# Kernel optimization log

Hardware: AMD Instinct MI355X
Metric: run time of the kernel (lower is better)

Reference implementation:

```python
import jax, jax.numpy as jnp
import numpy as np

B, S, H, N = 512, 50, 512, 20000


def setup_inputs() -> dict:
    key = jax.random.key(0)
    ks = jax.random.split(key, 8)
    sc = 1.0 / np.sqrt(H)
    return {
        "all_memory": jax.random.normal(ks[0], (B, S, H), jnp.float32),
        "last_memory": jax.random.normal(ks[1], (B, H), jnp.float32),
        "item_seq": jax.random.randint(ks[2], (B, S), 0, N),
        "mask": jnp.zeros((B, S), dtype=bool),
        "U_w": jax.random.normal(ks[3], (H, H), jnp.float32) * sc,
        "W_w": jax.random.normal(ks[4], (H, H), jnp.float32) * sc,
        "V_w": jax.random.normal(ks[5], (H,), jnp.float32) * sc,
        "V_b": jnp.zeros((1,), jnp.float32),
        "E_w": jax.random.normal(ks[6], (N, 2 * H), jnp.float32) * sc,
    }


def reference(all_memory, last_memory, item_seq, mask, U_w, W_w, V_w, V_b, E_w):
    # Additive (Bahdanau) attention over the basket-sequence memory.
    # torch nn.Linear computes x @ W.T (dropout is identity at eval).
    am = jnp.einsum('bsh,kh->bsk', all_memory, U_w)          # U_explore(all_memory)
    lm = last_memory @ W_w.T                                  # W_explore(last_memory)
    scores = jnp.tanh(am + lm[:, None, :]) @ V_w + V_b[0]     # [B, S]
    scores = jnp.where(mask, -1e9, scores)                    # masked_fill_
    alpha = jax.nn.softmax(scores, axis=1)                    # softmax over seq dim
    ctx = jnp.einsum('bs,bsh->bh', alpha, all_memory)         # attention readout
    feat = jnp.concatenate([ctx, last_memory], axis=-1)       # [B, 2H]
    logits = feat @ E_w.T                                     # [B, N] big GEMM
    # explore_mask = bmm((item_seq>0), one_hot(item_seq)) == scatter-add of counts
    counts = jnp.zeros((B, N), jnp.float32).at[
        jnp.arange(B)[:, None], item_seq
    ].add((item_seq > 0).astype(jnp.float32))
    logits = jnp.where(counts > 0, -jnp.inf, logits)          # mask seen items
    return jax.nn.sigmoid(logits)                             # sigmoid(-inf) -> 0
```

## Files before the change

### kernel.cpp

```cpp
#include <hip/hip_runtime.h>
#include <hip/hip_bf16.h>

#define Bdim 512
#define Sdim 50
#define Hdim 512
#define Ndim 20000
#define Kdim2 1024
#define SEENW 640

typedef __bf16 bf16x8 __attribute__((ext_vector_type(8)));
typedef float f32x4 __attribute__((ext_vector_type(4)));
typedef unsigned short u16;

__device__ __forceinline__ u16 f2bf(float f) {
  unsigned u = __builtin_bit_cast(unsigned, f);
  u = (u + 0x7fffu + ((u >> 16) & 1u)) >> 16;
  return (u16)u;
}
__device__ __forceinline__ float bf2f(u16 v) {
  unsigned u = ((unsigned)v) << 16;
  return __builtin_bit_cast(float, u);
}
__device__ __forceinline__ unsigned cvt_pk_bf16(float lo, float hi) {
  unsigned r;
  asm("v_cvt_pk_bf16_f32 %0, %1, %2" : "=v"(r) : "v"(lo), "v"(hi));
  return r;
}
__device__ __forceinline__ bf16x8 pack8(float4 lo, float4 hi) {
  union { unsigned u[4]; bf16x8 v; } r;
  r.u[0] = cvt_pk_bf16(lo.x, lo.y);
  r.u[1] = cvt_pk_bf16(lo.z, lo.w);
  r.u[2] = cvt_pk_bf16(hi.x, hi.y);
  r.u[3] = cvt_pk_bf16(hi.z, hi.w);
  return r.v;
}

__global__ __launch_bounds__(256) void prep_kernel(const float* __restrict__ a, u16* __restrict__ da,
                                                   const float* __restrict__ b, u16* __restrict__ db,
                                                   const float* __restrict__ c, u16* __restrict__ dc,
                                                   float* __restrict__ scores, float* __restrict__ lm,
                                                   unsigned* __restrict__ seen) {
  int i = blockIdx.x * blockDim.x + threadIdx.x;
  float4 v; ushort4 o;
  v = reinterpret_cast<const float4*>(a)[i];
  o.x = f2bf(v.x); o.y = f2bf(v.y); o.z = f2bf(v.z); o.w = f2bf(v.w);
  reinterpret_cast<ushort4*>(da)[i] = o;
  v = reinterpret_cast<const float4*>(b)[i];
  o.x = f2bf(v.x); o.y = f2bf(v.y); o.z = f2bf(v.z); o.w = f2bf(v.w);
  reinterpret_cast<ushort4*>(db)[i] = o;
  v = reinterpret_cast<const float4*>(c)[i];
  o.x = f2bf(v.x); o.y = f2bf(v.y); o.z = f2bf(v.z); o.w = f2bf(v.w);
  reinterpret_cast<ushort4*>(dc)[i] = o;
  int stride = gridDim.x * blockDim.x;
  for (int j = i; j < Bdim * Sdim; j += stride) scores[j] = 0.f;
  for (int j = i; j < Bdim * Hdim; j += stride) lm[j] = 0.f;
  for (int j = i; j < Bdim * SEENW; j += stride) seen[j] = 0u;
}

__global__ __launch_bounds__(256) void scatter_kernel(const int* __restrict__ iseq,
                                                      unsigned* __restrict__ seen) {
  int i = blockIdx.x * blockDim.x + threadIdx.x;
  if (i < Bdim * Sdim) {
    int b = i / Sdim;
    int it = iseq[i];
    if (it > 0) atomicOr(&seen[b * SEENW + (it >> 5)], 1u << (it & 31));
  }
}

__global__ __launch_bounds__(256) void softmax_ctx_kernel(
    const float* __restrict__ scores, const unsigned char* __restrict__ mask,
    const float* __restrict__ amF, const float* __restrict__ last_memory,
    u16* __restrict__ feat) {
  int b = blockIdx.x;
  __shared__ float alpha[Sdim];
  int tid = threadIdx.x;
  if (tid < 64) {
    float s = -1e30f;
    if (tid < Sdim) {
      s = scores[b * Sdim + tid];
      if (mask[b * Sdim + tid]) s = -1e9f;
    }
    float m = s;
#pragma unroll
    for (int off = 32; off; off >>= 1) m = fmaxf(m, __shfl_xor(m, off));
    float e = (tid < Sdim) ? __expf(s - m) : 0.f;
    float sum = e;
#pragma unroll
    for (int off = 32; off; off >>= 1) sum += __shfl_xor(sum, off);
    if (tid < Sdim) alpha[tid] = e / sum;
  }
  __syncthreads();
  for (int h = tid; h < Hdim; h += 256) {
    const float* amp = amF + ((long)b * Sdim) * Hdim + h;
    float c = 0.f;
#pragma unroll 5
    for (int s = 0; s < Sdim; ++s) c += alpha[s] * amp[(long)s * Hdim];
    feat[b * Kdim2 + h] = f2bf(c);
    feat[b * Kdim2 + Hdim + h] = f2bf(last_memory[b * Hdim + h]);
  }
}

#define BM 256
#define BN 128
#define BK 32

template <int EPI>
__global__ __launch_bounds__(512, 4) void gemm_bt(
    const u16* __restrict__ A, const u16* __restrict__ Bmat,
    const float* __restrict__ Af, const float* __restrict__ Bf,
    int M, int N, int K,
    float* __restrict__ out,
    const float* __restrict__ lm, const float* __restrict__ Vw,
    float* __restrict__ scores, const unsigned* __restrict__ seen) {
  __shared__ bf16x8 Asl[2][BM * BK / 8];
  __shared__ bf16x8 Bsl[2][BN * BK / 8];
  const int tid = threadIdx.x;
  const int lane = tid & 63;
  const int wid = tid >> 6;
  const int wr = wid >> 1, wc = wid & 1;
  const int la = lane & 15, lb = lane >> 4;

  int bx, by, kt0, kt1;
  if constexpr (EPI == 0) {
    bx = blockIdx.x; by = blockIdx.y;
    int ktotal = K / BK; int kper = ktotal / gridDim.z;
    kt0 = blockIdx.z * kper; kt1 = kt0 + kper;
  } else {
    int nwg = gridDim.x, bid = blockIdx.x;
    int q = nwg >> 3, r = nwg & 7;
    int x = bid & 7, i = bid >> 3;
    int wgid = (x < r ? x * (q + 1) : r * (q + 1) + (x - r) * q) + i;
    if constexpr (EPI == 1) { by = wgid >> 2; bx = wgid & 3; }
    else                    { bx = wgid >> 1; by = wgid & 1; }
    kt0 = 0; kt1 = K / BK;
  }
  const int m0 = by * BM;
  const int n0 = bx * BN;

  f32x4 acc[4][4];
  const f32x4 zero = {0.f, 0.f, 0.f, 0.f};
#pragma unroll
  for (int i = 0; i < 4; ++i)
#pragma unroll
    for (int j = 0; j < 4; ++j) acc[i][j] = zero;

  const int rw = tid >> 2;
  const int eA = (tid & 3) * 8;
  const int ch = tid & 3;
  int brB = n0 + rw; if (brB > N - 1) brB = N - 1;

  const u16 *gA0 = nullptr, *gA1 = nullptr, *gB = nullptr;
  const float *gAf0 = nullptr, *gAf1 = nullptr, *gBf = nullptr;
  if constexpr (EPI == 1) {
    gAf0 = Af + (long)(m0 + rw) * K + eA;
    gAf1 = Af + (long)(m0 + 128 + rw) * K + eA;
  } else {
    gA0 = A + (long)(m0 + rw) * K + eA;
    gA1 = A + (long)(m0 + 128 + rw) * K + eA;
  }
  if constexpr (EPI == 2) {
    gBf = Bf + (long)brB * K + eA;
  } else {
    gB = Bmat + (long)brB * K + eA;
  }

  float4 ra0, ra1, ra2, ra3;
  float4 rb0, rb1;

  auto STAGE_G = [&](int buf, int kt) {
    const int k0 = kt * BK;
    if constexpr (EPI != 1) {
      __builtin_amdgcn_global_load_lds((const __attribute__((address_space(1))) void*)(gA0 + k0),
                                       (__attribute__((address_space(3))) void*)(void*)&Asl[buf][wid * 64], 16, 0, 0);
      __builtin_amdgcn_global_load_lds((const __attribute__((address_space(1))) void*)(gA1 + k0),
                                       (__attribute__((address_space(3))) void*)(void*)&Asl[buf][512 + wid * 64], 16, 0, 0);
    }
    if constexpr (EPI != 2) {
      __builtin_amdgcn_global_load_lds((const __attribute__((address_space(1))) void*)(gB + k0),
                                       (__attribute__((address_space(3))) void*)(void*)&Bsl[buf][wid * 64], 16, 0, 0);
    }
  };
  auto LOADR = [&](int kt) {
    const int k0 = kt * BK;
    if constexpr (EPI == 1) {
      ra0 = *reinterpret_cast<const float4*>(gAf0 + k0);
      ra1 = *reinterpret_cast<const float4*>(gAf0 + k0 + 4);
      ra2 = *reinterpret_cast<const float4*>(gAf1 + k0);
      ra3 = *reinterpret_cast<const float4*>(gAf1 + k0 + 4);
    }
    if constexpr (EPI == 2) {
      rb0 = *reinterpret_cast<const float4*>(gBf + k0);
      rb1 = *reinterpret_cast<const float4*>(gBf + k0 + 4);
    }
  };
  auto WRITER = [&](int buf) {
    if constexpr (EPI == 1) {
      Asl[buf][rw * 4 + ch] = pack8(ra0, ra1);
      Asl[buf][(128 + rw) * 4 + ch] = pack8(ra2, ra3);
    }
    if constexpr (EPI == 2) {
      Bsl[buf][rw * 4 + ch] = pack8(rb0, rb1);
    }
  };

  STAGE_G(0, kt0);
  LOADR(kt0);
  WRITER(0);
  __syncthreads();
  int cur = 0;
  for (int kt = kt0; kt < kt1; ++kt) {
    const bool pf = (kt + 1 < kt1);
    if (pf) { STAGE_G(cur ^ 1, kt + 1); LOADR(kt + 1); }

    bf16x8 af[4], bfr[4];
#pragma unroll
    for (int mi = 0; mi < 4; ++mi)
      af[mi] = Asl[cur][(wr * 64 + mi * 16 + la) * 4 + lb];
#pragma unroll
    for (int ni = 0; ni < 4; ++ni)
      bfr[ni] = Bsl[cur][(wc * 64 + ni * 16 + la) * 4 + lb];
#pragma unroll
    for (int mi = 0; mi < 4; ++mi)
#pragma unroll
      for (int ni = 0; ni < 4; ++ni)
        acc[mi][ni] = __builtin_amdgcn_mfma_f32_16x16x32_bf16(af[mi], bfr[ni], acc[mi][ni], 0, 0, 0);

    if (pf) WRITER(cur ^ 1);
    __syncthreads();
    cur ^= 1;
  }

  if constexpr (EPI == 0) {
#pragma unroll
    for (int mi = 0; mi < 4; ++mi)
#pragma unroll
      for (int i = 0; i < 4; ++i) {
        int r = m0 + wr * 64 + mi * 16 + lb * 4 + i;
#pragma unroll
        for (int ni = 0; ni < 4; ++ni) {
          int c = n0 + wc * 64 + ni * 16 + la;
          atomicAdd(&out[(long)r * N + c], acc[mi][ni][i]);
        }
      }
  }
  if constexpr (EPI == 1) {
#pragma unroll
    for (int mi = 0; mi < 4; ++mi)
#pragma unroll
      for (int i = 0; i < 4; ++i) {
        int r = m0 + wr * 64 + mi * 16 + lb * 4 + i;
        int bidx = r / Sdim;
        float p = 0.f;
#pragma unroll
        for (int ni = 0; ni < 4; ++ni) {
          int c = n0 + wc * 64 + ni * 16 + la;
          float x = acc[mi][ni][i] + lm[bidx * Hdim + c];
          x = fminf(fmaxf(x, -9.f), 9.f);
          float e = __expf(2.f * x);
          p += Vw[c] * ((e - 1.f) / (e + 1.f));
        }
        p += __shfl_xor(p, 1);
        p += __shfl_xor(p, 2);
        p += __shfl_xor(p, 4);
        p += __shfl_xor(p, 8);
        if (la == 0) atomicAdd(&scores[r], p);
      }
  }
  if constexpr (EPI == 2) {
#pragma unroll
    for (int mi = 0; mi < 4; ++mi)
#pragma unroll
      for (int i = 0; i < 4; ++i) {
        int r = m0 + wr * 64 + mi * 16 + lb * 4 + i;
        long rb = (long)r * Ndim;
#pragma unroll
        for (int ni = 0; ni < 4; ++ni) {
          int c = n0 + wc * 64 + ni * 16 + la;
          if (c < Ndim) {
            unsigned wbits = seen[r * SEENW + (c >> 5)];
            float val = 0.f;
            if (!((wbits >> (c & 31)) & 1u))
              val = 1.f / (1.f + __expf(-acc[mi][ni][i]));
            out[rb + c] = val;
          }
        }
      }
  }
}

extern "C" void kernel_launch(void* const* d_in, const int* in_sizes, int n_in,
                              void* d_out, int out_size, void* d_ws, size_t ws_size,
                              hipStream_t stream) {
  (void)in_sizes; (void)n_in; (void)out_size; (void)ws_size;
  const float* all_memory  = (const float*)d_in[0];
  const float* last_memory = (const float*)d_in[1];
  const int*   item_seq    = (const int*)d_in[2];
  const unsigned char* mask = (const unsigned char*)d_in[3];
  const float* U_w = (const float*)d_in[4];
  const float* W_w = (const float*)d_in[5];
  const float* V_w = (const float*)d_in[6];
  const float* E_w = (const float*)d_in[8];
  float* out = (float*)d_out;

  char* w = (char*)d_ws;
  u16* wsFeat = (u16*)w; w += (size_t)Bdim * Kdim2 * 2;
  u16* wsLast = (u16*)w; w += (size_t)Hdim * Hdim * 2;
  u16* wsW    = (u16*)w; w += (size_t)Hdim * Hdim * 2;
  u16* wsU    = (u16*)w; w += (size_t)Hdim * Hdim * 2;
  float* wsLm     = (float*)w; w += (size_t)Bdim * Hdim * 4;
  float* wsScores = (float*)w; w += (size_t)Bdim * Sdim * 4;
  unsigned* wsSeen = (unsigned*)w; w += (size_t)Bdim * SEENW * 4;

  prep_kernel<<<256, 256, 0, stream>>>(last_memory, wsLast, W_w, wsW, U_w, wsU,
                                       wsScores, wsLm, wsSeen);
  scatter_kernel<<<100, 256, 0, stream>>>(item_seq, wsSeen);

  gemm_bt<0><<<dim3(Hdim / BN, Bdim / BM, 4), 512, 0, stream>>>(
      wsLast, wsW, nullptr, nullptr, Bdim, Hdim, Hdim, wsLm,
      nullptr, nullptr, nullptr, nullptr);
  gemm_bt<1><<<dim3((Bdim * Sdim / BM) * (Hdim / BN)), 512, 0, stream>>>(
      nullptr, wsU, all_memory, nullptr, Bdim * Sdim, Hdim, Hdim, nullptr,
      wsLm, V_w, wsScores, nullptr);
  softmax_ctx_kernel<<<Bdim, 256, 0, stream>>>(wsScores, mask, all_memory, last_memory, wsFeat);
  gemm_bt<2><<<dim3(((Ndim + BN - 1) / BN) * (Bdim / BM)), 512, 0, stream>>>(
      wsFeat, nullptr, nullptr, E_w, Bdim, Ndim, Kdim2, out,
      nullptr, nullptr, nullptr, wsSeen);
}
```

Baseline: 131.7 us.

## Add dedicated swizzled, triple-buffered pipelined kernel for the logits GEMM

The big logits GEMM moves out of the generic template into a dedicated kernel. A is staged through three LDS buffers via global_load_lds, and the fp32 E_w row loads are issued two iterations ahead in registers. The LDS chunk index is XOR-swizzled to reduce bank conflicts, and waits use explicit vmcnt/barrier control with sched_barriers. This aims to hide global-load latency and LDS conflicts, at the cost of more LDS and registers (launch bounds lowered to 2 blocks per SM).

After: 120.9 us. -8.1%, faster.

```diff
diff --git a/kernel.cpp b/kernel.cpp
--- a/kernel.cpp
+++ b/kernel.cpp
@@ -11,6 +11,9 @@
 typedef __bf16 bf16x8 __attribute__((ext_vector_type(8)));
 typedef float f32x4 __attribute__((ext_vector_type(4)));
 typedef unsigned short u16;
+
+#define AS1 __attribute__((address_space(1)))
+#define AS3 __attribute__((address_space(3)))
 
 __device__ __forceinline__ u16 f2bf(float f) {
   unsigned u = __builtin_bit_cast(unsigned, f);
@@ -107,11 +110,11 @@
 template <int EPI>
 __global__ __launch_bounds__(512, 4) void gemm_bt(
     const u16* __restrict__ A, const u16* __restrict__ Bmat,
-    const float* __restrict__ Af, const float* __restrict__ Bf,
+    const float* __restrict__ Af,
     int M, int N, int K,
     float* __restrict__ out,
     const float* __restrict__ lm, const float* __restrict__ Vw,
-    float* __restrict__ scores, const unsigned* __restrict__ seen) {
+    float* __restrict__ scores) {
   __shared__ bf16x8 Asl[2][BM * BK / 8];
   __shared__ bf16x8 Bsl[2][BN * BK / 8];
   const int tid = threadIdx.x;
@@ -130,8 +133,7 @@
     int q = nwg >> 3, r = nwg & 7;
     int x = bid & 7, i = bid >> 3;
     int wgid = (x < r ? x * (q + 1) : r * (q + 1) + (x - r) * q) + i;
-    if constexpr (EPI == 1) { by = wgid >> 2; bx = wgid & 3; }
-    else                    { bx = wgid >> 1; by = wgid & 1; }
+    by = wgid >> 2; bx = wgid & 3;
     kt0 = 0; kt1 = K / BK;
   }
   const int m0 = by * BM;
@@ -150,7 +152,7 @@
   int brB = n0 + rw; if (brB > N - 1) brB = N - 1;
 
   const u16 *gA0 = nullptr, *gA1 = nullptr, *gB = nullptr;
-  const float *gAf0 = nullptr, *gAf1 = nullptr, *gBf = nullptr;
+  const float *gAf0 = nullptr, *gAf1 = nullptr;
   if constexpr (EPI == 1) {
     gAf0 = Af + (long)(m0 + rw) * K + eA;
     gAf1 = Af + (long)(m0 + 128 + rw) * K + eA;
@@ -158,27 +160,20 @@
     gA0 = A + (long)(m0 + rw) * K + eA;
     gA1 = A + (long)(m0 + 128 + rw) * K + eA;
   }
-  if constexpr (EPI == 2) {
-    gBf = Bf + (long)brB * K + eA;
-  } else {
-    gB = Bmat + (long)brB * K + eA;
-  }
+  gB = Bmat + (long)brB * K + eA;
 
   float4 ra0, ra1, ra2, ra3;
-  float4 rb0, rb1;
 
   auto STAGE_G = [&](int buf, int kt) {
     const int k0 = kt * BK;
     if constexpr (EPI != 1) {
-      __builtin_amdgcn_global_load_lds((const __attribute__((address_space(1))) void*)(gA0 + k0),
-                                       (__attribute__((address_space(3))) void*)(void*)&Asl[buf][wid * 64], 16, 0, 0);
-      __builtin_amdgcn_global_load_lds((const __attribute__((address_space(1))) void*)(gA1 + k0),
-                                       (__attribute__((address_space(3))) void*)(void*)&Asl[buf][512 + wid * 64], 16, 0, 0);
+      __builtin_amdgcn_global_load_lds((const AS1 void*)(gA0 + k0),
+                                       (AS3 void*)(void*)&Asl[buf][wid * 64], 16, 0, 0);
+      __builtin_amdgcn_global_load_lds((const AS1 void*)(gA1 + k0),
+                                       (AS3 void*)(void*)&Asl[buf][512 + wid * 64], 16, 0, 0);
     }
-    if constexpr (EPI != 2) {
-      __builtin_amdgcn_global_load_lds((const __attribute__((address_space(1))) void*)(gB + k0),
-                                       (__attribute__((address_space(3))) void*)(void*)&Bsl[buf][wid * 64], 16, 0, 0);
-    }
+    __builtin_amdgcn_global_load_lds((const AS1 void*)(gB + k0),
+                                     (AS3 void*)(void*)&Bsl[buf][wid * 64], 16, 0, 0);
   };
   auto LOADR = [&](int kt) {
     const int k0 = kt * BK;
@@ -188,18 +183,11 @@
       ra2 = *reinterpret_cast<const float4*>(gAf1 + k0);
       ra3 = *reinterpret_cast<const float4*>(gAf1 + k0 + 4);
     }
-    if constexpr (EPI == 2) {
-      rb0 = *reinterpret_cast<const float4*>(gBf + k0);
-      rb1 = *reinterpret_cast<const float4*>(gBf + k0 + 4);
-    }
   };
   auto WRITER = [&](int buf) {
     if constexpr (EPI == 1) {
       Asl[buf][rw * 4 + ch] = pack8(ra0, ra1);
       Asl[buf][(128 + rw) * 4 + ch] = pack8(ra2, ra3);
-    }
-    if constexpr (EPI == 2) {
-      Bsl[buf][rw * 4 + ch] = pack8(rb0, rb1);
     }
   };
 
@@ -266,26 +254,125 @@
         if (la == 0) atomicAdd(&scores[r], p);
       }
   }
-  if constexpr (EPI == 2) {
-#pragma unroll
-    for (int mi = 0; mi < 4; ++mi)
-#pragma unroll
-      for (int i = 0; i < 4; ++i) {
-        int r = m0 + wr * 64 + mi * 16 + lb * 4 + i;
-        long rb = (long)r * Ndim;
-#pragma unroll
-        for (int ni = 0; ni < 4; ++ni) {
-          int c = n0 + wc * 64 + ni * 16 + la;
-          if (c < Ndim) {
-            unsigned wbits = seen[r * SEENW + (c >> 5)];
-            float val = 0.f;
-            if (!((wbits >> (c & 31)) & 1u))
-              val = 1.f / (1.f + __expf(-acc[mi][ni][i]));
-            out[rb + c] = val;
-          }
+}
+
+#define LBM 256
+#define LBN 128
+#define LBK 32
+
+__global__ __launch_bounds__(512, 2) void gemm_logits(
+    const u16* __restrict__ A, const float* __restrict__ Bf,
+    float* __restrict__ out, const unsigned* __restrict__ seen) {
+  __shared__ bf16x8 Asl[3][LBM * LBK / 8];
+  __shared__ bf16x8 Bsl[2][LBN * LBK / 8];
+  const int tid = threadIdx.x;
+  const int lane = tid & 63;
+  const int wid = tid >> 6;
+  const int wr = wid >> 1, wc = wid & 1;
+  const int la = lane & 15, lb = lane >> 4;
+  const int kch = lb ^ (la & 3);
+  const int K = Kdim2;
+  const int NT = K / LBK;
+
+  int nwg = gridDim.x, bid = blockIdx.x;
+  int q = nwg >> 3, r = nwg & 7;
+  int x = bid & 7, i0 = bid >> 3;
+  int wgid = (x < r ? x * (q + 1) : r * (q + 1) + (x - r) * q) + i0;
+  const int bx = wgid >> 1, by = wgid & 1;
+  const int m0 = by * LBM, n0 = bx * LBN;
+
+  f32x4 acc[4][4];
+  const f32x4 zero = {0.f, 0.f, 0.f, 0.f};
+#pragma unroll
+  for (int i = 0; i < 4; ++i)
+#pragma unroll
+    for (int j = 0; j < 4; ++j) acc[i][j] = zero;
+
+  const int rw = tid >> 2;
+  const int ch = tid & 3;
+  const int swz = ch ^ (rw & 3);
+  const int chs = swz;
+  int brB = n0 + rw; if (brB > Ndim - 1) brB = Ndim - 1;
+  const u16* gA0 = A + (long)(m0 + rw) * K + swz * 8;
+  const u16* gA1 = A + (long)(m0 + 128 + rw) * K + swz * 8;
+  const float* gBf = Bf + (long)brB * K + ch * 8;
+
+  auto STAGE_A = [&](int kt, int slot) {
+    const int k0 = kt * LBK;
+    __builtin_amdgcn_global_load_lds((const AS1 void*)(gA0 + k0),
+                                     (AS3 void*)(void*)&Asl[slot][wid * 64], 16, 0, 0);
+    __builtin_amdgcn_global_load_lds((const AS1 void*)(gA1 + k0),
+                                     (AS3 void*)(void*)&Asl[slot][512 + wid * 64], 16, 0, 0);
+  };
+  auto COMP = [&](int slA, int slB) {
+    bf16x8 af[4], bfr[4];
+#pragma unroll
+    for (int mi = 0; mi < 4; ++mi)
+      af[mi] = Asl[slA][(wr * 64 + mi * 16 + la) * 4 + kch];
+#pragma unroll
+    for (int ni = 0; ni < 4; ++ni)
+      bfr[ni] = Bsl[slB][(wc * 64 + ni * 16 + la) * 4 + kch];
+#pragma unroll
+    for (int mi = 0; mi < 4; ++mi)
+#pragma unroll
+      for (int ni = 0; ni < 4; ++ni)
+        acc[mi][ni] = __builtin_amdgcn_mfma_f32_16x16x32_bf16(af[mi], bfr[ni], acc[mi][ni], 0, 0, 0);
+  };
+
+  float4 b0lo, b0hi, b1lo, b1hi;
+
+  STAGE_A(0, 0);
+  __builtin_amdgcn_sched_barrier(0);
+  b0lo = *reinterpret_cast<const float4*>(gBf);
+  b0hi = *reinterpret_cast<const float4*>(gBf + 4);
+  __builtin_amdgcn_sched_barrier(0);
+  STAGE_A(1, 1);
+  __builtin_amdgcn_sched_barrier(0);
+  b1lo = *reinterpret_cast<const float4*>(gBf + LBK);
+  b1hi = *reinterpret_cast<const float4*>(gBf + LBK + 4);
+  Bsl[0][rw * 4 + chs] = pack8(b0lo, b0hi);
+  asm volatile("s_waitcnt vmcnt(4) lgkmcnt(0)" ::: "memory");
+  __builtin_amdgcn_sched_barrier(0);
+  __builtin_amdgcn_s_barrier();
+  __builtin_amdgcn_sched_barrier(0);
+
+  auto ITER = [&](int kt, float4& ldlo, float4& ldhi, float4& stlo, float4& sthi) {
+    int tpf = kt + 2; if (tpf > NT - 1) tpf = NT - 1;
+    STAGE_A(tpf, (kt + 2) % 3);
+    __builtin_amdgcn_sched_barrier(0);
+    ldlo = *reinterpret_cast<const float4*>(gBf + tpf * LBK);
+    ldhi = *reinterpret_cast<const float4*>(gBf + tpf * LBK + 4);
+    COMP(kt % 3, kt & 1);
+    Bsl[(kt + 1) & 1][rw * 4 + chs] = pack8(stlo, sthi);
+    asm volatile("s_waitcnt vmcnt(4) lgkmcnt(0)" ::: "memory");
+    __builtin_amdgcn_sched_barrier(0);
+    __builtin_amdgcn_s_barrier();
+    __builtin_amdgcn_sched_barrier(0);
+  };
+
+  for (int kt = 0; kt < NT; kt += 2) {
+    ITER(kt,     b0lo, b0hi, b1lo, b1hi);
+    ITER(kt + 1, b1lo, b1hi, b0lo, b0hi);
+  }
+
+#pragma unroll
+  for (int mi = 0; mi < 4; ++mi)
+#pragma unroll
+    for (int i = 0; i < 4; ++i) {
+      int r = m0 + wr * 64 + mi * 16 + lb * 4 + i;
+      long rb = (long)r * Ndim;
+#pragma unroll
+      for (int ni = 0; ni < 4; ++ni) {
+        int c = n0 + wc * 64 + ni * 16 + la;
+        if (c < Ndim) {
+          unsigned wbits = seen[r * SEENW + (c >> 5)];
+          float val = 0.f;
+          if (!((wbits >> (c & 31)) & 1u))
+            val = 1.f / (1.f + __expf(-acc[mi][ni][i]));
+          out[rb + c] = val;
         }
       }
-  }
+    }
 }
 
 extern "C" void kernel_launch(void* const* d_in, const int* in_sizes, int n_in,
@@ -316,13 +403,11 @@
   scatter_kernel<<<100, 256, 0, stream>>>(item_seq, wsSeen);
 
   gemm_bt<0><<<dim3(Hdim / BN, Bdim / BM, 4), 512, 0, stream>>>(
-      wsLast, wsW, nullptr, nullptr, Bdim, Hdim, Hdim, wsLm,
-      nullptr, nullptr, nullptr, nullptr);
+      wsLast, wsW, nullptr, Bdim, Hdim, Hdim, wsLm, nullptr, nullptr, nullptr);
   gemm_bt<1><<<dim3((Bdim * Sdim / BM) * (Hdim / BN)), 512, 0, stream>>>(
-      nullptr, wsU, all_memory, nullptr, Bdim * Sdim, Hdim, Hdim, nullptr,
-      wsLm, V_w, wsScores, nullptr);
+      nullptr, wsU, all_memory, Bdim * Sdim, Hdim, Hdim, nullptr,
+      wsLm, V_w, wsScores);
   softmax_ctx_kernel<<<Bdim, 256, 0, stream>>>(wsScores, mask, all_memory, last_memory, wsFeat);
-  gemm_bt<2><<<dim3(((Ndim + BN - 1) / BN) * (Bdim / BM)), 512, 0, stream>>>(
-      wsFeat, nullptr, nullptr, E_w, Bdim, Ndim, Kdim2, out,
-      nullptr, nullptr, nullptr, wsSeen);
-}
+  gemm_logits<<<dim3(((Ndim + LBN - 1) / LBN) * (Bdim / LBM)), 512, 0, stream>>>(
+      wsFeat, E_w, out, wsSeen);
+}
```
